# Kernel tuning notes

Measured on AMD Instinct MI355X. Metric: run time of the kernel, lower is better.

## Reference

```python
import jax, jax.numpy as jnp
import numpy as np

D_MODEL, D_INNER, D_STATE, DT_RANK, D_CONV = 768, 1536, 16, 48, 4
B, L = 2, 2048


def setup_inputs() -> dict:
    key = jax.random.key(0)
    ks = jax.random.split(key, 8)
    s = 0.02
    return {
        "x": jax.random.normal(ks[0], (B, L, D_MODEL), jnp.float32),
        "norm_w": jnp.ones((D_MODEL,), jnp.float32),
        "in_proj_w": jax.random.normal(ks[1], (2 * D_INNER, D_MODEL), jnp.float32) * s,
        "conv_w": jax.random.normal(ks[2], (D_INNER, 1, D_CONV), jnp.float32) * s,
        "conv_b": jnp.zeros((D_INNER,), jnp.float32),
        "x_proj_w": jax.random.normal(ks[3], (DT_RANK + 2 * D_STATE, D_INNER), jnp.float32) * s,
        "dt_proj_w": jax.random.normal(ks[4], (D_INNER, DT_RANK), jnp.float32) * s,
        "dt_proj_b": jax.random.normal(ks[5], (D_INNER,), jnp.float32) * s,
        "A_log": jnp.broadcast_to(jnp.log(jnp.arange(1, D_STATE + 1, dtype=jnp.float32)), (D_INNER, D_STATE)).copy(),
        "D": jnp.ones((D_INNER,), jnp.float32),
        "out_proj_w": jax.random.normal(ks[6], (D_MODEL, D_INNER), jnp.float32) * s,
    }


def _mamba_block(x, norm_w, in_proj_w, conv_w, conv_b, x_proj_w,
                 dt_proj_w, dt_proj_b, A_log, D, out_proj_w):
    residual = x
    # RMSNorm
    h = x * jax.lax.rsqrt(jnp.mean(x * x, axis=-1, keepdims=True) + 1e-5) * norm_w
    # in_proj -> chunk into (hs, gate)
    xz = jnp.einsum('bld,ed->ble', h, in_proj_w)          # [B,L,2*Di]
    xh, z = jnp.split(xz, 2, axis=-1)                     # each [B,L,Di]
    # causal depthwise conv1d (kernel D_CONV) + SiLU
    xt = jnp.transpose(xh, (0, 2, 1))                     # [B,Di,L]
    xt = jnp.pad(xt, ((0, 0), (0, 0), (D_CONV - 1, 0)))
    xc = jax.lax.conv_general_dilated(xt, conv_w, (1,), 'VALID',
                                      feature_group_count=D_INNER)
    xc = jax.nn.silu(xc + conv_b[None, :, None])
    xc = jnp.transpose(xc, (0, 2, 1))                     # [B,L,Di]
    # x_proj -> (dt, B, C)
    proj = jnp.einsum('bld,ed->ble', xc, x_proj_w)        # [B,L,dt_rank+2N]
    dt, Bm, Cm = jnp.split(proj, [DT_RANK, DT_RANK + D_STATE], axis=-1)
    delta = jax.nn.softplus(jnp.einsum('blr,dr->bld', dt, dt_proj_w) + dt_proj_b)  # [B,L,Di]
    A = -jnp.exp(A_log)                                   # [Di,N]
    dA = jnp.exp(delta[..., None] * A)                    # [B,L,Di,N]
    dBx = delta[..., None] * Bm[:, :, None, :] * xc[..., None]  # [B,L,Di,N]
    # selective scan over the sequence axis
    def step(hst, inp):
        dA_t, dBx_t, C_t = inp                            # [B,Di,N],[B,Di,N],[B,N]
        hst = dA_t * hst + dBx_t
        y = jnp.einsum('bdn,bn->bd', hst, C_t)
        return hst, y
    h0 = jnp.zeros((x.shape[0], D_INNER, D_STATE), x.dtype)
    _, ys = jax.lax.scan(step, h0, (jnp.moveaxis(dA, 1, 0),
                                    jnp.moveaxis(dBx, 1, 0),
                                    jnp.moveaxis(Cm, 1, 0)))
    y = jnp.moveaxis(ys, 0, 1)                            # [B,L,Di]
    y = y + xc * D                                        # skip connection D
    y = y * jax.nn.silu(z)                                # gate
    out = jnp.einsum('bld,ed->ble', y, out_proj_w)        # [B,L,Dm]
    return residual + out, residual


def reference(x, norm_w, in_proj_w, conv_w, conv_b, x_proj_w,
              dt_proj_w, dt_proj_b, A_log, D, out_proj_w):
    return _mamba_block(x, norm_w, in_proj_w, conv_w, conv_b, x_proj_w,
                        dt_proj_w, dt_proj_b, A_log, D, out_proj_w)
```

## Files before the change

kernel.cpp:

```cpp
#include <hip/hip_runtime.h>
#include <cstdint>
#include <cstddef>

typedef __bf16 bf16_t;
typedef __bf16 bf16x8 __attribute__((ext_vector_type(8)));
typedef float  f32x4  __attribute__((ext_vector_type(4)));

#define D_MODEL 768
#define D_INNER 1536
#define D_STATE 16
#define DT_RANK 48
#define NB      2
#define SEQ     2048
#define NTOK    (NB*SEQ)
#define XPROJ_N (DT_RANK + 2*D_STATE)
#define LC      64
#define NCHUNK  (SEQ/LC)
#define XP_KS   4
#define XP_KC   (D_INNER/XP_KS)

#define N_INW (2*D_INNER*D_MODEL)
#define N_XPW (XPROJ_N*D_INNER)
#define N_DTW (D_INNER*DT_RANK)
#define N_OPW (D_MODEL*D_INNER)
#define N_CVT (N_INW+N_XPW+N_DTW+N_OPW)
#define CVT_BLOCKS (N_CVT/1024)

typedef __attribute__((address_space(1))) void gvoid_t;
typedef __attribute__((address_space(3))) void lvoid_t;
__device__ __forceinline__ void g2lds16(const bf16_t* g, bf16_t* l) {
    __builtin_amdgcn_global_load_lds((gvoid_t*)g, (lvoid_t*)l, 16, 0, 0);
}

__global__ __launch_bounds__(256)
void prep_kernel(const float* __restrict__ in_proj_w, bf16_t* __restrict__ w_in,
                 const float* __restrict__ x_proj_w,  bf16_t* __restrict__ w_xp,
                 const float* __restrict__ dt_proj_w, bf16_t* __restrict__ w_dt,
                 const float* __restrict__ out_proj_w,bf16_t* __restrict__ w_op,
                 const float* __restrict__ x, const float* __restrict__ norm_w,
                 bf16_t* __restrict__ h, float* __restrict__ proj,
                 float* __restrict__ out0, float* __restrict__ out1) {
    const int blk = blockIdx.x;
    const int tid = threadIdx.x;
    if (blk < CVT_BLOCKS) {
        int off = (blk * 256 + tid) * 4;
        const float* s; bf16_t* d;
        if (off < N_INW) { s = in_proj_w + off; d = w_in + off; }
        else if ((off -= N_INW) < N_XPW) { s = x_proj_w + off; d = w_xp + off; }
        else if ((off -= N_XPW) < N_DTW) { s = dt_proj_w + off; d = w_dt + off; }
        else { off -= N_DTW; s = out_proj_w + off; d = w_op + off; }
        float4 v = *(const float4*)s;
        d[0] = (bf16_t)v.x; d[1] = (bf16_t)v.y;
        d[2] = (bf16_t)v.z; d[3] = (bf16_t)v.w;
        return;
    }
    int t = blk - CVT_BLOCKS;
    if (tid < XPROJ_N) proj[(size_t)t * XPROJ_N + tid] = 0.f;
    const float* xr = x + (size_t)t * D_MODEL;
    float v[3];
    float ss = 0.f;
#pragma unroll
    for (int i = 0; i < 3; i++) { v[i] = xr[tid + 256*i]; ss += v[i]*v[i]; }
#pragma unroll
    for (int off = 32; off >= 1; off >>= 1) ss += __shfl_down(ss, off);
    __shared__ float red[4];
    int lane = tid & 63, wv = tid >> 6;
    if (lane == 0) red[wv] = ss;
    __syncthreads();
    float tot = red[0] + red[1] + red[2] + red[3];
    float r = rsqrtf(tot * (1.f/(float)D_MODEL) + 1e-5f);
#pragma unroll
    for (int i = 0; i < 3; i++) {
        size_t idx = (size_t)t*D_MODEL + tid + 256*i;
        h[idx] = (bf16_t)(v[i] * r * norm_w[tid + 256*i]);
        out0[idx] = v[i];
        out1[idx] = v[i];
    }
}

__global__ __launch_bounds__(256)
void gemm_nt128(const bf16_t* __restrict__ A, int lda,
                const bf16_t* __restrict__ B, int ldb,
                bf16_t* __restrict__ C, int ldc, int K) {
    __shared__ __align__(16) bf16_t As[2][128*32];
    __shared__ __align__(16) bf16_t Bs[2][128*32];
    const int tid = threadIdx.x;
    const int wave = tid >> 6, lane = tid & 63;
    const int quad = lane >> 4, l16 = lane & 15;
    const int nbx = gridDim.x, nby = gridDim.y;
    int bid = blockIdx.y * nbx + blockIdx.x;
    const int cpx = (nbx * nby) >> 3;
    bid = (bid & 7) * cpx + (bid >> 3);
    const int m0 = (bid / nby) * 128, n0 = (bid % nby) * 128;
    const int wr = (wave >> 1) * 64, wc = (wave & 1) * 64;

    const int s0 = tid, s1 = tid + 256;
    const int r0 = s0 >> 2, q0 = ((s0 & 3) ^ ((r0 >> 1) & 3)) << 3;
    const int r1 = s1 >> 2, q1 = ((s1 & 3) ^ ((r1 >> 1) & 3)) << 3;

    const bf16_t* Ar0 = A + (size_t)(m0 + r0)*lda + q0;
    const bf16_t* Ar1 = A + (size_t)(m0 + r1)*lda + q1;
    const bf16_t* Br0 = B + (size_t)(n0 + r0)*ldb + q0;
    const bf16_t* Br1 = B + (size_t)(n0 + r1)*ldb + q1;

    f32x4 acc[4][4] = {};
    const int nit = K >> 5;

    g2lds16(Ar0, &As[0][wave*512]);
    g2lds16(Ar1, &As[0][wave*512 + 2048]);
    g2lds16(Br0, &Bs[0][wave*512]);
    g2lds16(Br1, &Bs[0][wave*512 + 2048]);

    for (int it = 0; it < nit; it++) {
        __syncthreads();
        if (it + 1 < nit) {
            int k = (it + 1) << 5;
            int nb = (it + 1) & 1;
            g2lds16(Ar0 + k, &As[nb][wave*512]);
            g2lds16(Ar1 + k, &As[nb][wave*512 + 2048]);
            g2lds16(Br0 + k, &Bs[nb][wave*512]);
            g2lds16(Br1 + k, &Bs[nb][wave*512 + 2048]);
        }
        const int buf = it & 1;
        bf16x8 af[4], bfr[4];
#pragma unroll
        for (int i = 0; i < 4; i++) {
            int rr = wr + i*16 + l16;
            af[i] = *(const bf16x8*)&As[buf][rr*32 + ((quad ^ ((rr >> 1) & 3)) << 3)];
        }
#pragma unroll
        for (int j = 0; j < 4; j++) {
            int rr = wc + j*16 + l16;
            bfr[j] = *(const bf16x8*)&Bs[buf][rr*32 + ((quad ^ ((rr >> 1) & 3)) << 3)];
        }
#pragma unroll
        for (int i = 0; i < 4; i++)
#pragma unroll
            for (int j = 0; j < 4; j++)
                acc[i][j] = __builtin_amdgcn_mfma_f32_16x16x32_bf16(af[i], bfr[j], acc[i][j], 0, 0, 0);
    }

#pragma unroll
    for (int i = 0; i < 4; i++)
#pragma unroll
        for (int j = 0; j < 4; j++) {
            int n = n0 + wc + j*16 + l16;
#pragma unroll
            for (int rr = 0; rr < 4; rr++) {
                int m = m0 + wr + i*16 + quad*4 + rr;
                C[(size_t)m * ldc + n] = (bf16_t)acc[i][j][rr];
            }
        }
}

__global__ __launch_bounds__(256)
void gemm_op(const bf16_t* __restrict__ A, const bf16_t* __restrict__ B,
             float* __restrict__ C) {
    __shared__ __align__(16) bf16_t As[2][128*32];
    __shared__ __align__(16) bf16_t Bs[2][128*32];
    const int tid = threadIdx.x;
    const int wave = tid >> 6, lane = tid & 63;
    const int quad = lane >> 4, l16 = lane & 15;
    const int nbx = gridDim.x, nby = gridDim.y;
    int bid = blockIdx.y * nbx + blockIdx.x;
    const int cpx = (nbx * nby) >> 3;
    bid = (bid & 7) * cpx + (bid >> 3);
    const int m0 = (bid / nby) * 128, n0 = (bid % nby) * 128;
    const int kbase = blockIdx.z * (D_INNER/2);
    const int wr = (wave >> 1) * 64, wc = (wave & 1) * 64;

    const int s0 = tid, s1 = tid + 256;
    const int r0 = s0 >> 2, q0 = ((s0 & 3) ^ ((r0 >> 1) & 3)) << 3;
    const int r1 = s1 >> 2, q1 = ((s1 & 3) ^ ((r1 >> 1) & 3)) << 3;

    const bf16_t* Ar0 = A + (size_t)(m0 + r0)*D_INNER + kbase + q0;
    const bf16_t* Ar1 = A + (size_t)(m0 + r1)*D_INNER + kbase + q1;
    const bf16_t* Br0 = B + (size_t)(n0 + r0)*D_INNER + kbase + q0;
    const bf16_t* Br1 = B + (size_t)(n0 + r1)*D_INNER + kbase + q1;

    f32x4 acc[4][4] = {};
    const int nit = (D_INNER/2) >> 5;

    g2lds16(Ar0, &As[0][wave*512]);
    g2lds16(Ar1, &As[0][wave*512 + 2048]);
    g2lds16(Br0, &Bs[0][wave*512]);
    g2lds16(Br1, &Bs[0][wave*512 + 2048]);

    for (int it = 0; it < nit; it++) {
        __syncthreads();
        if (it + 1 < nit) {
            int k = (it + 1) << 5;
            int nb = (it + 1) & 1;
            g2lds16(Ar0 + k, &As[nb][wave*512]);
            g2lds16(Ar1 + k, &As[nb][wave*512 + 2048]);
            g2lds16(Br0 + k, &Bs[nb][wave*512]);
            g2lds16(Br1 + k, &Bs[nb][wave*512 + 2048]);
        }
        const int buf = it & 1;
        bf16x8 af[4], bfr[4];
#pragma unroll
        for (int i = 0; i < 4; i++) {
            int rr = wr + i*16 + l16;
            af[i] = *(const bf16x8*)&As[buf][rr*32 + ((quad ^ ((rr >> 1) & 3)) << 3)];
        }
#pragma unroll
        for (int j = 0; j < 4; j++) {
            int rr = wc + j*16 + l16;
            bfr[j] = *(const bf16x8*)&Bs[buf][rr*32 + ((quad ^ ((rr >> 1) & 3)) << 3)];
        }
#pragma unroll
        for (int i = 0; i < 4; i++)
#pragma unroll
            for (int j = 0; j < 4; j++)
                acc[i][j] = __builtin_amdgcn_mfma_f32_16x16x32_bf16(af[i], bfr[j], acc[i][j], 0, 0, 0);
    }

#pragma unroll
    for (int i = 0; i < 4; i++)
#pragma unroll
        for (int j = 0; j < 4; j++) {
            int n = n0 + wc + j*16 + l16;
#pragma unroll
            for (int rr = 0; rr < 4; rr++) {
                int m = m0 + wr + i*16 + quad*4 + rr;
                unsafeAtomicAdd(&C[(size_t)m * D_MODEL + n], acc[i][j][rr]);
            }
        }
}

__global__ __launch_bounds__(256)
void gemm_xp(const bf16_t* __restrict__ A, const bf16_t* __restrict__ B,
             float* __restrict__ proj) {
    __shared__ __align__(16) bf16_t As[64*32];
    __shared__ __align__(16) bf16_t Bs[64*32];
    const int tid = threadIdx.x;
    const int m0 = blockIdx.x * 64, n0 = blockIdx.y * 64, kbase = blockIdx.z * XP_KC;
    const int r  = tid >> 2, p8 = (tid & 3) << 3;
    const int q8 = (((tid & 3) ^ ((r >> 1) & 3)) << 3);
    const int wave = tid >> 6, lane = tid & 63;
    const int quad = lane >> 4, l16 = lane & 15;

    f32x4 acc[4] = {{0.f,0.f,0.f,0.f},{0.f,0.f,0.f,0.f},
                    {0.f,0.f,0.f,0.f},{0.f,0.f,0.f,0.f}};

    for (int k0 = 0; k0 < XP_KC; k0 += 32) {
        int gk = kbase + k0 + q8;
        uint4 va = *(const uint4*)(A + (size_t)(m0 + r) * D_INNER + gk);
        *(uint4*)&As[r*32 + p8] = va;
        uint4 vb = {0u,0u,0u,0u};
        int nr = n0 + r;
        if (nr < XPROJ_N)
            vb = *(const uint4*)(B + (size_t)nr * D_INNER + gk);
        *(uint4*)&Bs[r*32 + p8] = vb;

        __syncthreads();
        int ra = wave*16 + l16;
        bf16x8 af = *(const bf16x8*)&As[ra*32 + ((quad ^ ((ra >> 1) & 3)) << 3)];
#pragma unroll
        for (int nt = 0; nt < 4; nt++) {
            int rb = nt*16 + l16;
            bf16x8 bfg = *(const bf16x8*)&Bs[rb*32 + ((quad ^ ((rb >> 1) & 3)) << 3)];
            acc[nt] = __builtin_amdgcn_mfma_f32_16x16x32_bf16(af, bfg, acc[nt], 0, 0, 0);
        }
        __syncthreads();
    }

#pragma unroll
    for (int nt = 0; nt < 4; nt++) {
        int n = n0 + nt*16 + l16;
        if (n >= XPROJ_N) continue;
#pragma unroll
        for (int rr = 0; rr < 4; rr++) {
            int m = m0 + wave*16 + quad*4 + rr;
            unsafeAtomicAdd(&proj[(size_t)m * XPROJ_N + n], acc[nt][rr]);
        }
    }
}

__global__ __launch_bounds__(192)
void conv_silu_kernel(const bf16_t* __restrict__ xz,
                      const float* __restrict__ cw,
                      const float* __restrict__ cb,
                      bf16_t* __restrict__ xc) {
    const int t0 = blockIdx.x * 8;
    const int l0 = t0 & (SEQ - 1);
    const int d = threadIdx.x * 8;

    float cwf[32];
#pragma unroll
    for (int q = 0; q < 8; q++)
        *(float4*)&cwf[q*4] = *(const float4*)&cw[d*4 + q*4];

    float cbv[8];
    *(float4*)&cbv[0] = *(const float4*)&cb[d];
    *(float4*)&cbv[4] = *(const float4*)&cb[d+4];

    bf16x8 rows[11];
#pragma unroll
    for (int r = 0; r < 11; r++) {
        if (l0 - 3 + r >= 0) {
            rows[r] = *(const bf16x8*)&xz[(size_t)(t0 - 3 + r) * (2*D_INNER) + d];
        } else {
#pragma unroll
            for (int i = 0; i < 8; i++) rows[r][i] = (bf16_t)0.f;
        }
    }

#pragma unroll
    for (int tt = 0; tt < 8; tt++) {
        float acc[8];
#pragma unroll
        for (int i = 0; i < 8; i++) acc[i] = cbv[i];
#pragma unroll
        for (int k = 0; k < 4; k++)
#pragma unroll
            for (int i = 0; i < 8; i++)
                acc[i] += (float)rows[tt + k][i] * cwf[i*4 + k];
        bf16x8 o;
#pragma unroll
        for (int i = 0; i < 8; i++) {
            float s = acc[i] / (1.f + __expf(-acc[i]));
            o[i] = (bf16_t)s;
        }
        *(bf16x8*)&xc[(size_t)(t0 + tt) * D_INNER + d] = o;
    }
}

__device__ __forceinline__ void delta_mfma(
    const float* __restrict__ proj, const bf16_t* __restrict__ w_dt,
    const float* __restrict__ bias, int bx, size_t tbase, int tid,
    bf16_t* As , bf16_t* Bs , bf16_t* Ds ) {
    const int wave = tid >> 6, lane = tid & 63;
    const int quad = lane >> 4, l16 = lane & 15;
    const int r  = tid >> 2;
    const int p8 = (tid & 3) << 3;
    const int x3 = ((tid & 3) ^ ((r >> 1) & 3)) << 3;

    f32x4 acc[4][4] = {};

#pragma unroll
    for (int kc = 0; kc < 2; kc++) {
        const int k0 = kc * 32;
        {
            int gk = k0 + x3;
            bf16x8 v;
            if (gk < DT_RANK) {
                const float* src = proj + (tbase + r) * XPROJ_N + gk;
                float4 f0 = *(const float4*)src;
                float4 f1 = *(const float4*)(src + 4);
                v[0]=(bf16_t)f0.x; v[1]=(bf16_t)f0.y; v[2]=(bf16_t)f0.z; v[3]=(bf16_t)f0.w;
                v[4]=(bf16_t)f1.x; v[5]=(bf16_t)f1.y; v[6]=(bf16_t)f1.z; v[7]=(bf16_t)f1.w;
            } else {
#pragma unroll
                for (int i = 0; i < 8; i++) v[i] = (bf16_t)0.f;
            }
            *(bf16x8*)&As[r*32 + p8] = v;
        }
#pragma unroll
        for (int it = 0; it < 4; it++) {
            int row = r + 64*it;
            uint4 vb = {0u,0u,0u,0u};
            if (k0 + x3 < DT_RANK)
                vb = *(const uint4*)(w_dt + (size_t)(bx*256 + row)*DT_RANK + k0 + x3);
            *(uint4*)&Bs[row*32 + p8] = vb;
        }
        __syncthreads();
        bf16x8 af[4];
#pragma unroll
        for (int mi = 0; mi < 4; mi++) {
            int rr = mi*16 + l16;
            af[mi] = *(const bf16x8*)&As[rr*32 + ((quad ^ ((rr >> 1) & 3)) << 3)];
        }
#pragma unroll
        for (int nj = 0; nj < 4; nj++) {
            int rb = wave*64 + nj*16 + l16;
            bf16x8 bfr = *(const bf16x8*)&Bs[rb*32 + ((quad ^ ((rb >> 1) & 3)) << 3)];
#pragma unroll
            for (int mi = 0; mi < 4; mi++)
                acc[mi][nj] = __builtin_amdgcn_mfma_f32_16x16x32_bf16(af[mi], bfr, acc[mi][nj], 0, 0, 0);
        }
        __syncthreads();
    }
#pragma unroll
    for (int nj = 0; nj < 4; nj++) {
        int dloc = wave*64 + nj*16 + l16;
        float b = bias[bx*256 + dloc];
#pragma unroll
        for (int mi = 0; mi < 4; mi++) {
#pragma unroll
            for (int rr2 = 0; rr2 < 4; rr2++) {
                int t = mi*16 + quad*4 + rr2;
                float u = acc[mi][nj][rr2] + b;
                float sp = (u > 20.f) ? u : log1pf(__expf(u));
                Ds[t*256 + dloc] = (bf16_t)sp;
            }
        }
    }
    __syncthreads();
}

__global__ __launch_bounds__(256)
void scan_part1(const bf16_t* __restrict__ xc,
                const float* __restrict__ proj,
                const bf16_t* __restrict__ w_dt,
                const float* __restrict__ dt_bias,
                const float* __restrict__ A_log,
                float* __restrict__ chunk_h, float* __restrict__ chunk_P) {
    __shared__ __align__(16) bf16_t uraw[64*256];
    bf16_t* As = uraw;
    bf16_t* Bs = uraw + 64*32;
    bf16_t* Ds = uraw;
    __shared__ float Bsv[LC][D_STATE];
    const int tid = threadIdx.x;
    const int bx = blockIdx.x;
    const int c = blockIdx.y, b = blockIdx.z;
    const size_t tbase = (size_t)b*SEQ + (size_t)c*LC;
    for (int i = tid; i < LC*D_STATE; i += 256) {
        int l = i >> 4, n = i & 15;
        Bsv[l][n] = proj[(tbase + l)*XPROJ_N + DT_RANK + n];
    }
    delta_mfma(proj, w_dt, dt_bias, bx, tbase, tid, As, Bs, Ds);

    const int d = bx*256 + tid;
    float Av2[D_STATE];
#pragma unroll
    for (int n = 0; n < D_STATE; n++)
        Av2[n] = -__expf(A_log[d*D_STATE + n]) * 1.44269504f;
    float s[D_STATE];
#pragma unroll
    for (int n = 0; n < D_STATE; n++) s[n] = 0.f;
    float sdv = 0.f;
    for (int l = 0; l < LC; l++) {
        float dv  = (float)Ds[l*256 + tid];
        float xcv = (float)xc[(tbase + l)*D_INNER + d];
        float dx = dv * xcv;
        sdv += dv;
#pragma unroll
        for (int n = 0; n < D_STATE; n++) {
            float a = __builtin_amdgcn_exp2f(dv * Av2[n]);
            s[n] = a * s[n] + dx * Bsv[l][n];
        }
    }
    size_t base = (((size_t)b*NCHUNK + c)*D_INNER + d)*D_STATE;
#pragma unroll
    for (int n = 0; n < D_STATE; n++) {
        chunk_h[base + n] = s[n];
        chunk_P[base + n] = __builtin_amdgcn_exp2f(Av2[n] * sdv);
    }
}

__global__ __launch_bounds__(256)
void scan_part2(float* __restrict__ chunk_h, const float* __restrict__ chunk_P) {
    int gid = blockIdx.x * 256 + threadIdx.x;
    int b  = gid / (D_INNER * D_STATE);
    int dn = gid - b * (D_INNER * D_STATE);
    const size_t cs = (size_t)D_INNER * D_STATE;
    size_t base = (size_t)b * NCHUNK * cs + dn;
    float H = 0.f;
    float S[8], P[8];
#pragma unroll
    for (int j = 0; j < 8; j++) {
        S[j] = chunk_h[base + (size_t)j * cs];
        P[j] = chunk_P[base + (size_t)j * cs];
    }
    for (int g = 0; g < NCHUNK/8; g++) {
        float S2[8], P2[8];
        if (g < NCHUNK/8 - 1) {
#pragma unroll
            for (int j = 0; j < 8; j++) {
                S2[j] = chunk_h[base + (size_t)((g+1)*8 + j) * cs];
                P2[j] = chunk_P[base + (size_t)((g+1)*8 + j) * cs];
            }
        }
#pragma unroll
        for (int j = 0; j < 8; j++) {
            size_t idx = base + (size_t)(g*8 + j) * cs;
            chunk_h[idx] = H;
            H = fmaf(P[j], H, S[j]);
        }
#pragma unroll
        for (int j = 0; j < 8; j++) { S[j] = S2[j]; P[j] = P2[j]; }
    }
}

__global__ __launch_bounds__(256)
void scan_part3(const bf16_t* __restrict__ xc,
                const float* __restrict__ proj,
                const bf16_t* __restrict__ w_dt,
                const float* __restrict__ dt_bias,
                const bf16_t* __restrict__ xz,
                const float* __restrict__ A_log,
                const float* __restrict__ Dw,
                const float* __restrict__ chunk_h,
                bf16_t* __restrict__ y) {
    __shared__ __align__(16) bf16_t uraw[64*256];
    bf16_t* As = uraw;
    bf16_t* Bs = uraw + 64*32;
    bf16_t* Ds = uraw;
    __shared__ float Bsv[LC][D_STATE];
    __shared__ float Csv[LC][D_STATE];
    const int tid = threadIdx.x;
    const int bx = blockIdx.x;
    const int c = blockIdx.y, b = blockIdx.z;
    const size_t tbase = (size_t)b*SEQ + (size_t)c*LC;
    for (int i = tid; i < LC*D_STATE; i += 256) {
        int l = i >> 4, n = i & 15;
        Bsv[l][n] = proj[(tbase + l)*XPROJ_N + DT_RANK + n];
        Csv[l][n] = proj[(tbase + l)*XPROJ_N + DT_RANK + D_STATE + n];
    }
    delta_mfma(proj, w_dt, dt_bias, bx, tbase, tid, As, Bs, Ds);

    const int d = bx*256 + tid;
    float Av2[D_STATE];
#pragma unroll
    for (int n = 0; n < D_STATE; n++)
        Av2[n] = -__expf(A_log[d*D_STATE + n]) * 1.44269504f;
    const float Dv = Dw[d];
    float s[D_STATE];
    size_t base = (((size_t)b*NCHUNK + c)*D_INNER + d)*D_STATE;
#pragma unroll
    for (int n = 0; n < D_STATE; n++) s[n] = chunk_h[base + n];
    for (int l = 0; l < LC; l++) {
        size_t t = tbase + l;
        float dv  = (float)Ds[l*256 + tid];
        float xcv = (float)xc[t*D_INNER + d];
        float dx = dv * xcv;
        float acc = 0.f;
#pragma unroll
        for (int n = 0; n < D_STATE; n++) {
            float a = __builtin_amdgcn_exp2f(dv * Av2[n]);
            s[n] = a * s[n] + dx * Bsv[l][n];
            acc += s[n] * Csv[l][n];
        }
        float zf = (float)xz[t*(2*D_INNER) + D_INNER + d];
        float g = zf / (1.f + __expf(-zf));
        y[t*D_INNER + d] = (bf16_t)((acc + xcv * Dv) * g);
    }
}

extern "C" void kernel_launch(void* const* d_in, const int* in_sizes, int n_in,
                              void* d_out, int out_size, void* d_ws, size_t ws_size,
                              hipStream_t stream) {
    const float* x          = (const float*)d_in[0];
    const float* norm_w     = (const float*)d_in[1];
    const float* in_proj_w  = (const float*)d_in[2];
    const float* conv_w     = (const float*)d_in[3];
    const float* conv_b     = (const float*)d_in[4];
    const float* x_proj_w   = (const float*)d_in[5];
    const float* dt_proj_w  = (const float*)d_in[6];
    const float* dt_proj_b  = (const float*)d_in[7];
    const float* A_log      = (const float*)d_in[8];
    const float* Dw         = (const float*)d_in[9];
    const float* out_proj_w = (const float*)d_in[10];

    float* out0 = (float*)d_out;
    float* out1 = out0 + (size_t)NTOK * D_MODEL;

    const size_t n_chunkst = (size_t)NB*NCHUNK*D_INNER*D_STATE;

    char* ws = (char*)d_ws;
    bf16_t* w_in  = (bf16_t*)ws;  ws += (size_t)N_INW * sizeof(bf16_t);
    bf16_t* w_xp  = (bf16_t*)ws;  ws += (size_t)N_XPW * sizeof(bf16_t);
    bf16_t* w_dt  = (bf16_t*)ws;  ws += (size_t)N_DTW * sizeof(bf16_t);
    bf16_t* w_op  = (bf16_t*)ws;  ws += (size_t)N_OPW * sizeof(bf16_t);
    bf16_t* h     = (bf16_t*)ws;  ws += (size_t)NTOK * D_MODEL   * sizeof(bf16_t);
    bf16_t* xz    = (bf16_t*)ws;  ws += (size_t)NTOK * 2*D_INNER * sizeof(bf16_t);
    bf16_t* xc    = (bf16_t*)ws;  ws += (size_t)NTOK * D_INNER   * sizeof(bf16_t);
    bf16_t* y     = (bf16_t*)ws;  ws += (size_t)NTOK * D_INNER   * sizeof(bf16_t);
    float*  proj  = (float*)ws;   ws += (size_t)NTOK * XPROJ_N   * sizeof(float);
    float*  ch    = (float*)ws;   ws += n_chunkst * sizeof(float);
    float*  cP    = (float*)ws;   ws += n_chunkst * sizeof(float);

    prep_kernel<<<CVT_BLOCKS + NTOK, 256, 0, stream>>>(
        in_proj_w, w_in, x_proj_w, w_xp, dt_proj_w, w_dt, out_proj_w, w_op,
        x, norm_w, h, proj, out0, out1);
    gemm_nt128<<<dim3(NTOK/128, (2*D_INNER)/128), 256, 0, stream>>>(
        h, D_MODEL, w_in, D_MODEL, xz, 2*D_INNER, D_MODEL);
    conv_silu_kernel<<<NTOK/8, 192, 0, stream>>>(xz, conv_w, conv_b, xc);
    gemm_xp<<<dim3(NTOK/64, 2, XP_KS), 256, 0, stream>>>(xc, w_xp, proj);
    scan_part1<<<dim3(D_INNER/256, NCHUNK, NB), 256, 0, stream>>>(
        xc, proj, w_dt, dt_proj_b, A_log, ch, cP);
    scan_part2<<<(int)((size_t)NB*D_INNER*D_STATE/256), 256, 0, stream>>>(ch, cP);
    scan_part3<<<dim3(D_INNER/256, NCHUNK, NB), 256, 0, stream>>>(
        xc, proj, w_dt, dt_proj_b, xz, A_log, Dw, ch, y);
    gemm_op<<<dim3(NTOK/128, D_MODEL/128, 2), 256, 0, stream>>>(y, w_op, out0);
}
```

Baseline: 316.4 us.

## Halve scan chunk length and batch per-step global loads in scan loops

Reduces the chunk length of the chunked selective scan from 64 to 32 tokens, doubling the number of chunks and thread blocks in the scan passes while shrinking per-block LDS and the delta MFMA tile. The scan loops now prefetch eight timesteps of delta, xc and z into registers before the recurrence to hide global load latency. In exchange, the serial inter-chunk pass and the chunk state buffers double in size, and the delta weight tile is loaded twice as often per token.

After: 294.3 us. 7.0% less time.

```diff
diff --git a/kernel.cpp b/kernel.cpp
--- a/kernel.cpp
+++ b/kernel.cpp
@@ -14,7 +14,7 @@
 #define SEQ     2048
 #define NTOK    (NB*SEQ)
 #define XPROJ_N (DT_RANK + 2*D_STATE)
-#define LC      64
+#define LC      32
 #define NCHUNK  (SEQ/LC)
 #define XP_KS   4
 #define XP_KC   (D_INNER/XP_KS)
@@ -326,7 +326,7 @@
     }
 }
 
-__device__ __forceinline__ void delta_mfma(
+__device__ __forceinline__ void delta_mfma32(
     const float* __restrict__ proj, const bf16_t* __restrict__ w_dt,
     const float* __restrict__ bias, int bx, size_t tbase, int tid,
     bf16_t* As , bf16_t* Bs , bf16_t* Ds ) {
@@ -336,12 +336,12 @@
     const int p8 = (tid & 3) << 3;
     const int x3 = ((tid & 3) ^ ((r >> 1) & 3)) << 3;
 
-    f32x4 acc[4][4] = {};
+    f32x4 acc[2][4] = {};
 
 #pragma unroll
     for (int kc = 0; kc < 2; kc++) {
         const int k0 = kc * 32;
-        {
+        if (r < 32) {
             int gk = k0 + x3;
             bf16x8 v;
             if (gk < DT_RANK) {
@@ -365,9 +365,9 @@
             *(uint4*)&Bs[row*32 + p8] = vb;
         }
         __syncthreads();
-        bf16x8 af[4];
-#pragma unroll
-        for (int mi = 0; mi < 4; mi++) {
+        bf16x8 af[2];
+#pragma unroll
+        for (int mi = 0; mi < 2; mi++) {
             int rr = mi*16 + l16;
             af[mi] = *(const bf16x8*)&As[rr*32 + ((quad ^ ((rr >> 1) & 3)) << 3)];
         }
@@ -376,7 +376,7 @@
             int rb = wave*64 + nj*16 + l16;
             bf16x8 bfr = *(const bf16x8*)&Bs[rb*32 + ((quad ^ ((rb >> 1) & 3)) << 3)];
 #pragma unroll
-            for (int mi = 0; mi < 4; mi++)
+            for (int mi = 0; mi < 2; mi++)
                 acc[mi][nj] = __builtin_amdgcn_mfma_f32_16x16x32_bf16(af[mi], bfr, acc[mi][nj], 0, 0, 0);
         }
         __syncthreads();
@@ -386,7 +386,7 @@
         int dloc = wave*64 + nj*16 + l16;
         float b = bias[bx*256 + dloc];
 #pragma unroll
-        for (int mi = 0; mi < 4; mi++) {
+        for (int mi = 0; mi < 2; mi++) {
 #pragma unroll
             for (int rr2 = 0; rr2 < 4; rr2++) {
                 int t = mi*16 + quad*4 + rr2;
@@ -406,9 +406,9 @@
                 const float* __restrict__ dt_bias,
                 const float* __restrict__ A_log,
                 float* __restrict__ chunk_h, float* __restrict__ chunk_P) {
-    __shared__ __align__(16) bf16_t uraw[64*256];
+    __shared__ __align__(16) bf16_t uraw[32*32 + 256*32];
     bf16_t* As = uraw;
-    bf16_t* Bs = uraw + 64*32;
+    bf16_t* Bs = uraw + 32*32;
     bf16_t* Ds = uraw;
     __shared__ float Bsv[LC][D_STATE];
     const int tid = threadIdx.x;
@@ -419,7 +419,7 @@
         int l = i >> 4, n = i & 15;
         Bsv[l][n] = proj[(tbase + l)*XPROJ_N + DT_RANK + n];
     }
-    delta_mfma(proj, w_dt, dt_bias, bx, tbase, tid, As, Bs, Ds);
+    delta_mfma32(proj, w_dt, dt_bias, bx, tbase, tid, As, Bs, Ds);
 
     const int d = bx*256 + tid;
     float Av2[D_STATE];
@@ -430,15 +430,25 @@
 #pragma unroll
     for (int n = 0; n < D_STATE; n++) s[n] = 0.f;
     float sdv = 0.f;
-    for (int l = 0; l < LC; l++) {
-        float dv  = (float)Ds[l*256 + tid];
-        float xcv = (float)xc[(tbase + l)*D_INNER + d];
-        float dx = dv * xcv;
-        sdv += dv;
-#pragma unroll
-        for (int n = 0; n < D_STATE; n++) {
-            float a = __builtin_amdgcn_exp2f(dv * Av2[n]);
-            s[n] = a * s[n] + dx * Bsv[l][n];
+    for (int g = 0; g < LC/8; g++) {
+        float dvv[8], xv[8];
+#pragma unroll
+        for (int j = 0; j < 8; j++) {
+            int l = g*8 + j;
+            dvv[j] = (float)Ds[l*256 + tid];
+            xv[j]  = (float)xc[(tbase + l)*D_INNER + d];
+        }
+#pragma unroll
+        for (int j = 0; j < 8; j++) {
+            int l = g*8 + j;
+            float dv = dvv[j];
+            float dx = dv * xv[j];
+            sdv += dv;
+#pragma unroll
+            for (int n = 0; n < D_STATE; n++) {
+                float a = __builtin_amdgcn_exp2f(dv * Av2[n]);
+                s[n] = a * s[n] + dx * Bsv[l][n];
+            }
         }
     }
     size_t base = (((size_t)b*NCHUNK + c)*D_INNER + d)*D_STATE;
@@ -493,9 +503,9 @@
                 const float* __restrict__ Dw,
                 const float* __restrict__ chunk_h,
                 bf16_t* __restrict__ y) {
-    __shared__ __align__(16) bf16_t uraw[64*256];
+    __shared__ __align__(16) bf16_t uraw[32*32 + 256*32];
     bf16_t* As = uraw;
-    bf16_t* Bs = uraw + 64*32;
+    bf16_t* Bs = uraw + 32*32;
     bf16_t* Ds = uraw;
     __shared__ float Bsv[LC][D_STATE];
     __shared__ float Csv[LC][D_STATE];
@@ -508,7 +518,7 @@
         Bsv[l][n] = proj[(tbase + l)*XPROJ_N + DT_RANK + n];
         Csv[l][n] = proj[(tbase + l)*XPROJ_N + DT_RANK + D_STATE + n];
     }
-    delta_mfma(proj, w_dt, dt_bias, bx, tbase, tid, As, Bs, Ds);
+    delta_mfma32(proj, w_dt, dt_bias, bx, tbase, tid, As, Bs, Ds);
 
     const int d = bx*256 + tid;
     float Av2[D_STATE];
@@ -520,21 +530,33 @@
     size_t base = (((size_t)b*NCHUNK + c)*D_INNER + d)*D_STATE;
 #pragma unroll
     for (int n = 0; n < D_STATE; n++) s[n] = chunk_h[base + n];
-    for (int l = 0; l < LC; l++) {
-        size_t t = tbase + l;
-        float dv  = (float)Ds[l*256 + tid];
-        float xcv = (float)xc[t*D_INNER + d];
-        float dx = dv * xcv;
-        float acc = 0.f;
-#pragma unroll
-        for (int n = 0; n < D_STATE; n++) {
-            float a = __builtin_amdgcn_exp2f(dv * Av2[n]);
-            s[n] = a * s[n] + dx * Bsv[l][n];
-            acc += s[n] * Csv[l][n];
-        }
-        float zf = (float)xz[t*(2*D_INNER) + D_INNER + d];
-        float g = zf / (1.f + __expf(-zf));
-        y[t*D_INNER + d] = (bf16_t)((acc + xcv * Dv) * g);
+    for (int g = 0; g < LC/8; g++) {
+        float dvv[8], xv[8], zv[8];
+#pragma unroll
+        for (int j = 0; j < 8; j++) {
+            int l = g*8 + j;
+            size_t t = tbase + l;
+            dvv[j] = (float)Ds[l*256 + tid];
+            xv[j]  = (float)xc[t*D_INNER + d];
+            zv[j]  = (float)xz[t*(2*D_INNER) + D_INNER + d];
+        }
+#pragma unroll
+        for (int j = 0; j < 8; j++) {
+            int l = g*8 + j;
+            float dv = dvv[j];
+            float xcv = xv[j];
+            float dx = dv * xcv;
+            float acc = 0.f;
+#pragma unroll
+            for (int n = 0; n < D_STATE; n++) {
+                float a = __builtin_amdgcn_exp2f(dv * Av2[n]);
+                s[n] = a * s[n] + dx * Bsv[l][n];
+                acc += s[n] * Csv[l][n];
+            }
+            float zf = zv[j];
+            float gt = zf / (1.f + __expf(-zf));
+            y[(tbase + l)*D_INNER + d] = (bf16_t)((acc + xcv * Dv) * gt);
+        }
     }
 }
 
```
